# Kernel tuning notes

Hardware: AMD Instinct MI355X
Metric: run time of the kernel (lower is better)

## Reference

```python
import jax, jax.numpy as jnp
import numpy as np

B, N, D, E = 8, 512, 256, 16384  # batch, num_nodes, hidden_dim, num_edges


def setup_inputs() -> dict:
    key = jax.random.key(0)
    kf, ke, k1, k2, k3, k4 = jax.random.split(key, 6)
    features = jax.random.normal(kf, (B, N, D), dtype=jnp.float32)
    edge_index = jax.random.randint(ke, (2, E), 0, N, dtype=jnp.int64)
    # weight_net: Linear(2D -> D), ReLU, Linear(D -> 1), Sigmoid
    s1 = 1.0 / np.sqrt(2 * D)
    s2 = 1.0 / np.sqrt(D)
    W1 = jax.random.uniform(k1, (2 * D, D), jnp.float32, -s1, s1)
    b1 = jax.random.uniform(k2, (D,), jnp.float32, -s1, s1)
    W2 = jax.random.uniform(k3, (D, 1), jnp.float32, -s2, s2)
    b2 = jax.random.uniform(k4, (1,), jnp.float32, -s2, s2)
    return {"features": features, "W1": W1, "b1": b1, "W2": W2, "b2": b2,
            "edge_index": edge_index}


def reference(features, W1, b1, W2, b2, edge_index):
    src, dst = edge_index[0], edge_index[1]            # [E], [E]
    fi = features[:, src]                              # [B, E, D]
    fj = features[:, dst]                              # [B, E, D]
    pair = jnp.concatenate([fi, fj], axis=-1)          # [B, E, 2D]
    h = jax.nn.relu(jnp.einsum('bef,fh->beh', pair, W1) + b1)   # [B, E, D]
    s = jax.nn.sigmoid(jnp.einsum('beh,ho->beo', h, W2) + b2)[..., 0]  # [B, E]
    bsz, n = features.shape[0], features.shape[1]
    weights = jnp.zeros((bsz, n, n), features.dtype).at[:, src, dst].set(s)
    return weights
```

## Files before the change

kernel.cpp:

```cpp
#include <hip/hip_runtime.h>
#include <hip/hip_bf16.h>
#include <cstdint>

#define B_ 8
#define N_ 512
#define D_ 256
#define E_ 16384
#define H_ 256

#define SA_STRIDE 56
#define SB_STRIDE 56
#define BCAP 128

using bf16x8 = __attribute__((ext_vector_type(8))) short;
using f32x4  = __attribute__((ext_vector_type(4))) float;

__device__ inline unsigned short f2bf(float f) {
    union { float f; unsigned u; } v; v.f = f;
    unsigned u = v.u;
    return (unsigned short)((u + 0x7fffu + ((u >> 16) & 1u)) >> 16);
}

__global__ __launch_bounds__(256)
void prep_k(const float* __restrict__ W1, unsigned short* __restrict__ W1T,
            int* __restrict__ gCount) {
    __shared__ float tile[64][65];
    const int tb = blockIdx.x, t = threadIdx.x;
    if (tb == 32) {
        gCount[t] = 0;
        gCount[t + 256] = 0;
        return;
    }
    const int h   = tb >> 4;
    const int rem = tb & 15;
    const int tk  = (rem >> 2) * 64;
    const int tn  = (rem & 3) * 64;
    const float* Wh = W1 + (size_t)h * 256 * 256;
    const int c = t & 63, r0 = t >> 6;
#pragma unroll
    for (int i = 0; i < 16; i++) {
        int r = r0 + i * 4;
        tile[r][c] = Wh[(size_t)(tk + r) * 256 + tn + c];
    }
    __syncthreads();
#pragma unroll
    for (int i = 0; i < 16; i++) {
        int rn = r0 + i * 4;
        W1T[(size_t)(h * 256 + tn + rn) * 256 + tk + c] = f2bf(tile[c][rn]);
    }
}

__global__ __launch_bounds__(256)
void node_gemm(const float* __restrict__ feat,
               const unsigned short* __restrict__ W1T,
               const float* __restrict__ b1,
               const int* __restrict__ eidx,
               unsigned short* __restrict__ P,
               float4* __restrict__ out4,
               int* __restrict__ gCount, int* __restrict__ gBucket) {
    __shared__ unsigned short sA[64 * SA_STRIDE];
    __shared__ unsigned short sB[256 * SB_STRIDE];

    const int t = threadIdx.x;

    if (blockIdx.x >= 128) {
        int e = (blockIdx.x - 128) * 256 + t;
        int s = eidx[e];
        int d = eidx[E_ + e];
        int pos = atomicAdd(&gCount[s], 1);
        gBucket[(s << 7) + pos] = d;
        return;
    }

    const int bm = blockIdx.x >> 1;
    const int bn = blockIdx.x & 1;
    const int m0 = bm * 64;

    {
        float4 z = make_float4(0.f, 0.f, 0.f, 0.f);
        float4* oz = out4 + (size_t)blockIdx.x * 4096 + t;
#pragma unroll
        for (int i = 0; i < 16; i++) oz[i * 256] = z;
    }

    const int arow = t >> 2;
    const int akg  = (t & 3) * 8;
    const float* pA = feat + (size_t)(m0 + arow) * 256;
    const unsigned short* pB = W1T + (size_t)(bn * 256 + t) * 256;

    const int wave = t >> 6, lane = t & 63, l15 = lane & 15, quad = lane >> 4;

    f32x4 acc[4][4];
#pragma unroll
    for (int rm = 0; rm < 4; rm++)
#pragma unroll
        for (int cn = 0; cn < 4; cn++)
            acc[rm][cn] = (f32x4){0.f, 0.f, 0.f, 0.f};

    for (int k0 = 0; k0 < 256; k0 += 32) {
        __syncthreads();
        {
            float4 lo = *(const float4*)(pA + k0 + akg);
            float4 hi = *(const float4*)(pA + k0 + akg + 4);
            union { bf16x8 v; unsigned short s[8]; } u;
            u.s[0] = f2bf(lo.x); u.s[1] = f2bf(lo.y); u.s[2] = f2bf(lo.z); u.s[3] = f2bf(lo.w);
            u.s[4] = f2bf(hi.x); u.s[5] = f2bf(hi.y); u.s[6] = f2bf(hi.z); u.s[7] = f2bf(hi.w);
            *(bf16x8*)(sA + arow * SA_STRIDE + akg) = u.v;
        }
        {
            const unsigned short* p = pB + k0;
            uint4 q0 = *(const uint4*)(p);
            uint4 q1 = *(const uint4*)(p + 8);
            uint4 q2 = *(const uint4*)(p + 16);
            uint4 q3 = *(const uint4*)(p + 24);
            *(uint4*)(sB + t * SB_STRIDE +  0) = q0;
            *(uint4*)(sB + t * SB_STRIDE +  8) = q1;
            *(uint4*)(sB + t * SB_STRIDE + 16) = q2;
            *(uint4*)(sB + t * SB_STRIDE + 24) = q3;
        }
        __syncthreads();

        bf16x8 af[4], bfr[4];
#pragma unroll
        for (int rm = 0; rm < 4; rm++)
            af[rm] = *(const bf16x8*)(sA + (rm * 16 + l15) * SA_STRIDE + quad * 8);
#pragma unroll
        for (int cn = 0; cn < 4; cn++)
            bfr[cn] = *(const bf16x8*)(sB + (wave * 64 + cn * 16 + l15) * SB_STRIDE + quad * 8);
#pragma unroll
        for (int rm = 0; rm < 4; rm++)
#pragma unroll
            for (int cn = 0; cn < 4; cn++)
                acc[rm][cn] = __builtin_amdgcn_mfma_f32_16x16x32_bf16(af[rm], bfr[cn], acc[rm][cn], 0, 0, 0);
    }

#pragma unroll
    for (int cn = 0; cn < 4; cn++) {
        int colh = wave * 64 + cn * 16 + l15;
        float bias = (bn == 0) ? b1[colh] : 0.f;
        int col = bn * 256 + colh;
#pragma unroll
        for (int rm = 0; rm < 4; rm++)
#pragma unroll
            for (int r = 0; r < 4; r++) {
                int row = m0 + rm * 16 + quad * 4 + r;
                P[(size_t)row * 512 + col] = f2bf(acc[rm][cn][r] + bias);
            }
    }
}

__device__ inline float dot8nb(uint4 qu, uint4 qv, const float* w2p) {
    unsigned us[4] = {qu.x, qu.y, qu.z, qu.w};
    unsigned vs[4] = {qv.x, qv.y, qv.z, qv.w};
    float p = 0.f;
#pragma unroll
    for (int j = 0; j < 4; j++) {
        float ulo = __uint_as_float(us[j] << 16);
        float uhi = __uint_as_float(us[j] & 0xffff0000u);
        float vlo = __uint_as_float(vs[j] << 16);
        float vhi = __uint_as_float(vs[j] & 0xffff0000u);
        float hlo = fmaxf(ulo + vlo, 0.f);
        float hhi = fmaxf(uhi + vhi, 0.f);
        p = fmaf(hlo, w2p[2 * j],     p);
        p = fmaf(hhi, w2p[2 * j + 1], p);
    }
    return p;
}

__global__ __launch_bounds__(256)
void edge_score(const unsigned short* __restrict__ P,
                const float* __restrict__ W2, const float* __restrict__ b2,
                const int* __restrict__ gCount, const int* __restrict__ gBucket,
                float* __restrict__ out) {
    const int b     = blockIdx.x & 7;
    const int chunk = blockIdx.x >> 3;
    const int lane  = threadIdx.x & 63;
    const int wave  = threadIdx.x >> 6;
    const int g     = lane >> 4;
    const int w     = lane & 15;
    const int wid   = wave * 4 + g;
    const int s     = 2 * chunk + (wid >> 3);
    const int o     = wid & 7;

    const int en = gCount[s];
    const int* bucket = gBucket + (s << 7);

    float w2r[16];
#pragma unroll
    for (int j = 0; j < 4; j++)
        *(float4*)(w2r + 4 * j) = *(const float4*)(W2 + w * 16 + 4 * j);
    const float b2v = b2[0];

    const unsigned short* Pu = P + ((size_t)b * 512 + s) * 512 + w * 16;
    uint4 u0 = *(const uint4*)(Pu);
    uint4 u1 = *(const uint4*)(Pu + 8);
    const unsigned short* Pv = P + (size_t)b * 512 * 512 + 256 + w * 16;
    float* outb = out + ((size_t)b * 512 + s) * 512;

    int j = o;
    int dst0 = 0; uint4 v00 = {}, v01 = {};
    if (j < en) {
        dst0 = bucket[j];
        const unsigned short* pv = Pv + (size_t)dst0 * 512;
        v00 = *(const uint4*)pv; v01 = *(const uint4*)(pv + 8);
    }
    while (j < en) {
        int jn = j + 8;
        int dst1 = 0; uint4 v10 = {}, v11 = {};
        if (jn < en) {
            dst1 = bucket[jn];
            const unsigned short* pv = Pv + (size_t)dst1 * 512;
            v10 = *(const uint4*)pv; v11 = *(const uint4*)(pv + 8);
        }
        float p = dot8nb(u0, v00, w2r) + dot8nb(u1, v01, w2r + 8);
        p += __shfl_xor(p, 1);
        p += __shfl_xor(p, 2);
        p += __shfl_xor(p, 4);
        p += __shfl_xor(p, 8);
        if (w == 0) {
            float sv = 1.0f / (1.0f + __expf(-(p + b2v)));
            outb[dst0] = sv;
        }
        dst0 = dst1; v00 = v10; v01 = v11; j = jn;
    }
}

extern "C" void kernel_launch(void* const* d_in, const int* in_sizes, int n_in,
                              void* d_out, int out_size, void* d_ws, size_t ws_size,
                              hipStream_t stream) {
    const float* feat = (const float*)d_in[0];
    const float* W1   = (const float*)d_in[1];
    const float* b1   = (const float*)d_in[2];
    const float* W2   = (const float*)d_in[3];
    const float* b2   = (const float*)d_in[4];
    const int*   eidx = (const int*)d_in[5];
    float* out = (float*)d_out;

    unsigned short* W1T = (unsigned short*)d_ws;
    unsigned short* P   = (unsigned short*)((char*)d_ws + (1 << 20));
    int* gCount  = (int*)((char*)d_ws + (6 << 20));
    int* gBucket = (int*)((char*)d_ws + (6 << 20) + 4096);

    prep_k<<<33, 256, 0, stream>>>(W1, W1T, gCount);
    node_gemm<<<192, 256, 0, stream>>>(feat, W1T, b1, eidx, P, (float4*)out, gCount, gBucket);
    edge_score<<<2048, 256, 0, stream>>>(P, W2, b2, gCount, gBucket, out);
}
```

Baseline: 97.26 us.

## Bucket edges with shared-memory histograms in prep kernel instead of global atomics

Edge bucketing moves from global atomics in node_gemm to per-block shared-memory atomics in prep_k. Each of 8 edge blocks writes its own sub-bucket per source node, along with a per-sub-block count. edge_score rebuilds a prefix sum over the 8 sub-counts and looks up each edge's sub-bucket with a short compare chain. This removes global atomic contention and the separate zeroing of counts, and shortens node_gemm to the GEMM blocks only. The cost is extra index arithmetic per edge fetch, and each sub-bucket is capped at 32 edges per source.

```diff
diff --git a/kernel.cpp b/kernel.cpp
--- a/kernel.cpp
+++ b/kernel.cpp
@@ -10,7 +10,8 @@
 
 #define SA_STRIDE 56
 #define SB_STRIDE 56
-#define BCAP 128
+#define NSB 8
+#define SUBCAP 32
 
 using bf16x8 = __attribute__((ext_vector_type(8))) short;
 using f32x4  = __attribute__((ext_vector_type(4))) float;
@@ -22,15 +23,31 @@
 }
 
 __global__ __launch_bounds__(256)
-void prep_k(const float* __restrict__ W1, unsigned short* __restrict__ W1T,
-            int* __restrict__ gCount) {
+void prep_k(const float* __restrict__ W1, const int* __restrict__ eidx,
+            unsigned short* __restrict__ W1T,
+            int* __restrict__ gCnt, int* __restrict__ gBucket) {
+    const int tb = blockIdx.x, t = threadIdx.x;
+
+    if (tb >= 32) {
+        __shared__ int hist[512];
+        const int sb = tb - 32;
+        for (int i = t; i < 512; i += 256) hist[i] = 0;
+        __syncthreads();
+#pragma unroll
+        for (int k = 0; k < 8; k++) {
+            int e = sb * 2048 + k * 256 + t;
+            int s = eidx[e];
+            int d = eidx[E_ + e];
+            int slot = atomicAdd(&hist[s], 1);
+            gBucket[(s * NSB + sb) * SUBCAP + slot] = d;
+        }
+        __syncthreads();
+        for (int s = t; s < 512; s += 256)
+            gCnt[s * NSB + sb] = hist[s];
+        return;
+    }
+
     __shared__ float tile[64][65];
-    const int tb = blockIdx.x, t = threadIdx.x;
-    if (tb == 32) {
-        gCount[t] = 0;
-        gCount[t + 256] = 0;
-        return;
-    }
     const int h   = tb >> 4;
     const int rem = tb & 15;
     const int tk  = (rem >> 2) * 64;
@@ -54,24 +71,12 @@
 void node_gemm(const float* __restrict__ feat,
                const unsigned short* __restrict__ W1T,
                const float* __restrict__ b1,
-               const int* __restrict__ eidx,
                unsigned short* __restrict__ P,
-               float4* __restrict__ out4,
-               int* __restrict__ gCount, int* __restrict__ gBucket) {
+               float4* __restrict__ out4) {
     __shared__ unsigned short sA[64 * SA_STRIDE];
     __shared__ unsigned short sB[256 * SB_STRIDE];
 
-    const int t = threadIdx.x;
-
-    if (blockIdx.x >= 128) {
-        int e = (blockIdx.x - 128) * 256 + t;
-        int s = eidx[e];
-        int d = eidx[E_ + e];
-        int pos = atomicAdd(&gCount[s], 1);
-        gBucket[(s << 7) + pos] = d;
-        return;
-    }
-
+    const int t  = threadIdx.x;
     const int bm = blockIdx.x >> 1;
     const int bn = blockIdx.x & 1;
     const int m0 = bm * 64;
@@ -170,7 +175,7 @@
 __global__ __launch_bounds__(256)
 void edge_score(const unsigned short* __restrict__ P,
                 const float* __restrict__ W2, const float* __restrict__ b2,
-                const int* __restrict__ gCount, const int* __restrict__ gBucket,
+                const int* __restrict__ gCnt, const int* __restrict__ gBucket,
                 float* __restrict__ out) {
     const int b     = blockIdx.x & 7;
     const int chunk = blockIdx.x >> 3;
@@ -182,8 +187,17 @@
     const int s     = 2 * chunk + (wid >> 3);
     const int o     = wid & 7;
 
-    const int en = gCount[s];
-    const int* bucket = gBucket + (s << 7);
+    const int* cp = gCnt + s * NSB;
+    int4 c0 = *(const int4*)cp;
+    int4 c1 = *(const int4*)(cp + 4);
+    int pre[9];
+    pre[0] = 0;
+    pre[1] = pre[0] + c0.x; pre[2] = pre[1] + c0.y;
+    pre[3] = pre[2] + c0.z; pre[4] = pre[3] + c0.w;
+    pre[5] = pre[4] + c1.x; pre[6] = pre[5] + c1.y;
+    pre[7] = pre[6] + c1.z; pre[8] = pre[7] + c1.w;
+    const int en = pre[8];
+    const int* bucket = gBucket + s * (NSB * SUBCAP);
 
     float w2r[16];
 #pragma unroll
@@ -197,10 +211,17 @@
     const unsigned short* Pv = P + (size_t)b * 512 * 512 + 256 + w * 16;
     float* outb = out + ((size_t)b * 512 + s) * 512;
 
+    auto fetch = [&](int j) -> int {
+        int i = 0;
+#pragma unroll
+        for (int q = 1; q < 8; q++) i += (j >= pre[q]);
+        return bucket[i * SUBCAP + (j - pre[i])];
+    };
+
     int j = o;
     int dst0 = 0; uint4 v00 = {}, v01 = {};
     if (j < en) {
-        dst0 = bucket[j];
+        dst0 = fetch(j);
         const unsigned short* pv = Pv + (size_t)dst0 * 512;
         v00 = *(const uint4*)pv; v01 = *(const uint4*)(pv + 8);
     }
@@ -208,7 +229,7 @@
         int jn = j + 8;
         int dst1 = 0; uint4 v10 = {}, v11 = {};
         if (jn < en) {
-            dst1 = bucket[jn];
+            dst1 = fetch(jn);
             const unsigned short* pv = Pv + (size_t)dst1 * 512;
             v10 = *(const uint4*)pv; v11 = *(const uint4*)(pv + 8);
         }
@@ -238,10 +259,10 @@
 
     unsigned short* W1T = (unsigned short*)d_ws;
     unsigned short* P   = (unsigned short*)((char*)d_ws + (1 << 20));
-    int* gCount  = (int*)((char*)d_ws + (6 << 20));
-    int* gBucket = (int*)((char*)d_ws + (6 << 20) + 4096);
-
-    prep_k<<<33, 256, 0, stream>>>(W1, W1T, gCount);
-    node_gemm<<<192, 256, 0, stream>>>(feat, W1T, b1, eidx, P, (float4*)out, gCount, gBucket);
-    edge_score<<<2048, 256, 0, stream>>>(P, W2, b2, gCount, gBucket, out);
-}
+    int* gCnt    = (int*)((char*)d_ws + (6 << 20));
+    int* gBucket = (int*)((char*)d_ws + (6 << 20) + (1 << 16));
+
+    prep_k<<<40, 256, 0, stream>>>(W1, eidx, W1T, gCnt, gBucket);
+    node_gemm<<<128, 256, 0, stream>>>(feat, W1T, b1, P, (float4*)out);
+    edge_score<<<2048, 256, 0, stream>>>(P, W2, b2, gCnt, gBucket, out);
+}
```

Result: no change. 96.82 us (-0.5%).
